# Performance work log

Measured on AMD Instinct MI355X. Metric: run time of the kernel, lower is better.

The kernel has to match this reference:

```python
import jax, jax.numpy as jnp
import numpy as np

N_NODES = 50000
N_EDGES = 800000
EMB = 128
HID = [128, 128]
OUT = 64
CE = 8  # stand-in for CROSS_ENTROPY_INDEXES: first 8 output columns get sigmoid


def _linear_params(key, d_in, d_out):
    k1, k2 = jax.random.split(key)
    s = 1.0 / np.sqrt(d_in)
    w = jax.random.uniform(k1, (d_in, d_out), minval=-s, maxval=s, dtype=jnp.float32)
    b = jax.random.uniform(k2, (d_out,), minval=-s, maxval=s, dtype=jnp.float32)
    return w, b


def setup_inputs() -> dict:
    key = jax.random.key(0)
    ks = jax.random.split(key, 16)
    z = jax.random.normal(ks[0], (N_NODES, EMB), dtype=jnp.float32)
    edge_index = jax.random.randint(ks[1], (2, N_EDGES), 0, N_NODES, dtype=jnp.int64)
    # SAGEConv params: neighbor weight (with bias) + root weight
    w1_n, b1 = _linear_params(ks[2], EMB, HID[0])
    w1_r, _ = _linear_params(ks[3], EMB, HID[0])
    w2_n, b2 = _linear_params(ks[4], HID[0], HID[1])
    w2_r, _ = _linear_params(ks[5], HID[0], HID[1])
    wf_n, bf = _linear_params(ks[6], HID[1], OUT)
    wf_r, _ = _linear_params(ks[7], HID[1], OUT)
    # initial residual linears: emb -> hid[1], emb -> out
    w_res1, b_res1 = _linear_params(ks[8], EMB, HID[1])
    w_res2, b_res2 = _linear_params(ks[9], EMB, OUT)
    return dict(z=z, edge_index=edge_index,
                w1_n=w1_n, w1_r=w1_r, b1=b1,
                w2_n=w2_n, w2_r=w2_r, b2=b2,
                wf_n=wf_n, wf_r=wf_r, bf=bf,
                w_res1=w_res1, b_res1=b_res1,
                w_res2=w_res2, b_res2=b_res2)


def _sage(x, src, dst, w_n, w_r, b, n_nodes):
    # mean-aggregate neighbor features at target nodes, then affine combine with root
    msg = x[src]                                        # [E, d]
    agg = jax.ops.segment_sum(msg, dst, num_segments=n_nodes)
    deg = jax.ops.segment_sum(jnp.ones_like(dst, dtype=x.dtype), dst, num_segments=n_nodes)
    mean = agg / jnp.maximum(deg, 1.0)[:, None]
    return mean @ w_n + x @ w_r + b


def reference(z, edge_index, w1_n, w1_r, b1, w2_n, w2_r, b2, wf_n, wf_r, bf,
              w_res1, b_res1, w_res2, b_res2):
    n = z.shape[0]
    src, dst = edge_index[0], edge_index[1]
    h = jax.nn.relu(_sage(z, src, dst, w1_n, w1_r, b1, n))
    # mid layer (dropout is identity in eval) + initial residual
    h = jax.nn.relu(_sage(h, src, dst, w2_n, w2_r, b2, n))
    h = h + (z @ w_res1 + b_res1)
    # final conv + final residual
    h = _sage(h, src, dst, wf_n, wf_r, bf, n)
    h = h + (z @ w_res2 + b_res2)
    # sigmoid on cross-entropy columns
    h = h.at[:, :CE].set(jax.nn.sigmoid(h[:, :CE]))
    return h
```

## Files before the change

### kernel.cpp

```cpp
#include <hip/hip_runtime.h>
#include <hip/hip_bf16.h>
#include <math.h>

#define NN 50000
#define NE 800000
#define NB 391
#define EPB 6250

typedef short bf16x8 __attribute__((ext_vector_type(8)));
typedef float f32x4 __attribute__((ext_vector_type(4)));
typedef unsigned short us4 __attribute__((ext_vector_type(4)));
typedef unsigned short us8 __attribute__((ext_vector_type(8)));
typedef unsigned int u32x4 __attribute__((ext_vector_type(4)));

__device__ __forceinline__ float bf2f(unsigned short u) {
  union { unsigned int i; float f; } x; x.i = ((unsigned int)u) << 16; return x.f;
}
__device__ __forceinline__ unsigned short f2bf(float f) {
  union { float f; unsigned int i; } x; x.f = f;
  unsigned int i = x.i;
  unsigned int r = i + 0x7FFF + ((i >> 16) & 1);
  return (unsigned short)(r >> 16);
}
__device__ __forceinline__ us4 pack4(f32x4 v) {
  us4 o; o[0] = f2bf(v[0]); o[1] = f2bf(v[1]); o[2] = f2bf(v[2]); o[3] = f2bf(v[3]);
  return o;
}

__global__ __launch_bounds__(256) void bhist_kernel(const int* __restrict__ dstn,
                                                    int* __restrict__ bhist) {
  __shared__ int h[NB];
  for (int i = threadIdx.x; i < NB; i += 256) h[i] = 0;
  __syncthreads();
  int e0 = blockIdx.x * EPB;
  for (int i = threadIdx.x; i < EPB; i += 256)
    atomicAdd(&h[dstn[e0 + i] >> 7], 1);
  __syncthreads();
  for (int i = threadIdx.x; i < NB; i += 256)
    if (h[i]) atomicAdd(&bhist[i], h[i]);
}

__global__ __launch_bounds__(512) void bscan_kernel(const int* __restrict__ bhist,
                                                    int* __restrict__ bucket_off,
                                                    int* __restrict__ gcur) {
  __shared__ int s[512];
  int t = threadIdx.x;
  int v = (t < NB) ? bhist[t] : 0;
  s[t] = v; __syncthreads();
  for (int off = 1; off < 512; off <<= 1) {
    int x = (t >= off) ? s[t - off] : 0;
    __syncthreads();
    s[t] += x;
    __syncthreads();
  }
  if (t < NB) { bucket_off[t] = s[t] - v; gcur[t] = 0; }
  if (t == NB - 1) bucket_off[NB] = s[t];
}

__global__ __launch_bounds__(256) void bscat_kernel(const int* __restrict__ srcn,
                                                    const int* __restrict__ dstn,
                                                    const int* __restrict__ bucket_off,
                                                    int* __restrict__ gcur,
                                                    unsigned long long* __restrict__ ebuf) {
  __shared__ int hist[NB];
  __shared__ int base[NB];
  for (int i = threadIdx.x; i < NB; i += 256) hist[i] = 0;
  __syncthreads();
  int e0 = blockIdx.x * EPB;
  for (int i = threadIdx.x; i < EPB; i += 256)
    atomicAdd(&hist[dstn[e0 + i] >> 7], 1);
  __syncthreads();
  for (int i = threadIdx.x; i < NB; i += 256) {
    int c = hist[i];
    base[i] = c ? (bucket_off[i] + atomicAdd(&gcur[i], c)) : 0;
  }
  __syncthreads();
  for (int i = threadIdx.x; i < EPB; i += 256) {
    int s = srcn[e0 + i], d = dstn[e0 + i];
    int b = d >> 7;
    int pos = atomicSub(&hist[b], 1) - 1;
    ebuf[(size_t)base[b] + pos] = ((unsigned long long)(unsigned)d << 32) | (unsigned)s;
  }
}

__global__ __launch_bounds__(256) void bfill_kernel(const unsigned long long* __restrict__ ebuf,
                                                    const int* __restrict__ bucket_off,
                                                    int* __restrict__ rowoff,
                                                    int* __restrict__ csr) {
  int b = blockIdx.x;
  int bo = bucket_off[b], cnt = bucket_off[b + 1] - bo;
  __shared__ int ndeg[128], noff[128];
  int t = threadIdx.x;
  if (t < 128) ndeg[t] = 0;
  __syncthreads();
  for (int i = t; i < cnt; i += 256)
    atomicAdd(&ndeg[(int)(ebuf[bo + i] >> 32) & 127], 1);
  __syncthreads();
  if (t < 128) noff[t] = ndeg[t];
  __syncthreads();
  for (int off = 1; off < 128; off <<= 1) {
    int x = 0;
    if (t < 128 && t >= off) x = noff[t - off];
    __syncthreads();
    if (t < 128 && t >= off) noff[t] += x;
    __syncthreads();
  }
  if (t < 128) {
    int ex = noff[t] - ndeg[t];
    noff[t] = ex;
    int node = b * 128 + t;
    if (node < NN) rowoff[node] = bo + ex;
  }
  if (b == NB - 1 && t == 0) rowoff[NN] = NE;
  __syncthreads();
  for (int i = t; i < cnt; i += 256) {
    unsigned long long e = ebuf[bo + i];
    int dl = (int)(e >> 32) & 127;
    int pos = atomicSub(&ndeg[dl], 1) - 1;
    csr[bo + noff[dl] + pos] = (int)(unsigned)e;
  }
}

__global__ void prep_kernel(const float* __restrict__ w1n, const float* __restrict__ w1r,
                            const float* __restrict__ w2n, const float* __restrict__ w2r,
                            const float* __restrict__ wfn, const float* __restrict__ wfr,
                            const float* __restrict__ wr1, const float* __restrict__ wr2,
                            unsigned short* __restrict__ Bp1, unsigned short* __restrict__ Bp2,
                            unsigned short* __restrict__ Bp3) {
  int g = blockIdx.x * 256 + threadIdx.x;
  unsigned short* D; int NT, fi;
  int which;
  if      (g < 10240) { fi = g;         D = Bp1; NT = 20; which = 1; }
  else if (g < 14336) { fi = g - 10240; D = Bp2; NT = 8;  which = 2; }
  else if (g < 16384) { fi = g - 14336; D = Bp3; NT = 4;  which = 3; }
  else return;
  int lane = fi & 63, t = fi >> 6;
  int nt = t % NT, k0i = t / NT;
  int m = lane & 15, q = lane >> 4;
  int kb = k0i * 32 + q * 8;
  int n = nt * 16 + m;
  int hi = (kb >= 128);
  int k0_ = kb - (hi ? 128 : 0);
  const float* W = nullptr; int Nseg = 128; int nn = n;
  if (which == 1) {
    if (n < 128)      { W = hi ? w1r : w1n; nn = n; Nseg = 128; }
    else if (n < 256) { W = hi ? wr1 : nullptr; nn = n - 128; Nseg = 128; }
    else              { W = hi ? wr2 : nullptr; nn = n - 256; Nseg = 64; }
  } else if (which == 2) { W = hi ? w2r : w2n; Nseg = 128; }
  else                   { W = hi ? wfr : wfn; Nseg = 64; }
  unsigned short o[8];
#pragma unroll
  for (int j = 0; j < 8; j++)
    o[j] = W ? f2bf(W[(size_t)(k0_ + j) * Nseg + nn]) : (unsigned short)0;
  *(us8*)(D + (size_t)fi * 8) = *(const us8*)o;
}

__global__ void convz_kernel(const float* __restrict__ z, unsigned short* __restrict__ A1) {
  int i = blockIdx.x * 256 + threadIdx.x;
  if (i >= NN * 128 / 4) return;
  int i4 = i * 4;
  int row = i4 >> 7, c = i4 & 127;
  float4 v = *(const float4*)(z + i4);
  us4 o = { f2bf(v.x), f2bf(v.y), f2bf(v.z), f2bf(v.w) };
  *(us4*)(A1 + (size_t)row * 256 + 128 + c) = o;
}

__global__ __launch_bounds__(256) void agg_kernel(const unsigned short* __restrict__ feat, int fstride,
                                                  unsigned short* __restrict__ outm, int ostride,
                                                  const int* __restrict__ rowoff,
                                                  const int* __restrict__ csr) {
  int wave = threadIdx.x >> 6, lane = threadIdx.x & 63;
  int node = blockIdx.x * 4 + wave;
  if (node >= NN) return;
  int beg = rowoff[node], end = rowoff[node + 1];
  int g = lane >> 4;
  int c = (lane & 15) << 3;
  float a[8];
#pragma unroll
  for (int i = 0; i < 8; i++) a[i] = 0.f;
  int j = beg + g;
  for (; j + 12 < end; j += 16) {
    int s0 = csr[j];
    int s1 = csr[j + 4];
    int s2 = csr[j + 8];
    int s3 = csr[j + 12];
    u32x4 v0 = *(const u32x4*)(feat + (size_t)s0 * fstride + c);
    u32x4 v1 = *(const u32x4*)(feat + (size_t)s1 * fstride + c);
    u32x4 v2 = *(const u32x4*)(feat + (size_t)s2 * fstride + c);
    u32x4 v3 = *(const u32x4*)(feat + (size_t)s3 * fstride + c);
#pragma unroll
    for (int i = 0; i < 4; i++) {
      a[2*i]   += bf2f((unsigned short)(v0[i] & 0xffff)) + bf2f((unsigned short)(v1[i] & 0xffff))
                + bf2f((unsigned short)(v2[i] & 0xffff)) + bf2f((unsigned short)(v3[i] & 0xffff));
      a[2*i+1] += bf2f((unsigned short)(v0[i] >> 16)) + bf2f((unsigned short)(v1[i] >> 16))
                + bf2f((unsigned short)(v2[i] >> 16)) + bf2f((unsigned short)(v3[i] >> 16));
    }
  }
  for (; j < end; j += 4) {
    int s0 = csr[j];
    u32x4 v0 = *(const u32x4*)(feat + (size_t)s0 * fstride + c);
#pragma unroll
    for (int i = 0; i < 4; i++) {
      a[2*i]   += bf2f((unsigned short)(v0[i] & 0xffff));
      a[2*i+1] += bf2f((unsigned short)(v0[i] >> 16));
    }
  }
#pragma unroll
  for (int i = 0; i < 8; i++) {
    a[i] += __shfl_xor(a[i], 16, 64);
    a[i] += __shfl_xor(a[i], 32, 64);
  }
  if (g == 0) {
    float inv = 1.f / fmaxf((float)(end - beg), 1.f);
    unsigned int o[4];
#pragma unroll
    for (int i = 0; i < 4; i++)
      o[i] = ((unsigned int)f2bf(a[2*i+1] * inv) << 16) | f2bf(a[2*i] * inv);
    *(u32x4*)(outm + (size_t)node * ostride + c) = *(const u32x4*)o;
  }
}

__global__ __launch_bounds__(256) void gemm1_kernel(
    const unsigned short* __restrict__ A,
    const unsigned short* __restrict__ Bp,
    const float* __restrict__ b1, const float* __restrict__ br1, const float* __restrict__ br2,
    unsigned short* __restrict__ h1out,
    unsigned short* __restrict__ res1, unsigned short* __restrict__ res2)
{
  const int NT = 20;
  int wave = threadIdx.x >> 6, lane = threadIdx.x & 63;
  int row0 = blockIdx.x * 64 + wave * 16;
  int m = lane & 15, q = lane >> 4;
  int ybase = blockIdx.y * 10;
  f32x4 acc[10];
#pragma unroll
  for (int i = 0; i < 10; i++) acc[i] = (f32x4){0.f, 0.f, 0.f, 0.f};
  const unsigned short* arow = A + (size_t)(row0 + m) * 256 + q * 8;
  bf16x8 af[8];
#pragma unroll
  for (int k0i = 0; k0i < 8; ++k0i) af[k0i] = *(const bf16x8*)(arow + k0i * 32);
#pragma unroll
  for (int k0i = 0; k0i < 8; ++k0i) {
    const unsigned short* bk = Bp + ((size_t)k0i * NT + ybase) * 512 + lane * 8;
#pragma unroll
    for (int s = 0; s < 10; ++s) {
      bf16x8 bfr = *(const bf16x8*)(bk + s * 512);
      acc[s] = __builtin_amdgcn_mfma_f32_16x16x32_bf16(bfr, af[k0i], acc[s], 0, 0, 0);
    }
  }
  int row = row0 + m;
  if (row >= NN) return;
  int cb = q * 4;
#pragma unroll
  for (int s = 0; s < 10; ++s) {
    int nt = ybase + s;
    f32x4 v = acc[s];
    if (nt < 8) {
      int col = nt * 16 + cb;
      float4 bb = *(const float4*)(b1 + col);
      v[0] = fmaxf(v[0] + bb.x, 0.f); v[1] = fmaxf(v[1] + bb.y, 0.f);
      v[2] = fmaxf(v[2] + bb.z, 0.f); v[3] = fmaxf(v[3] + bb.w, 0.f);
      *(us4*)(h1out + (size_t)row * 256 + col) = pack4(v);
    } else if (nt < 16) {
      int col = (nt - 8) * 16 + cb;
      float4 bb = *(const float4*)(br1 + col);
      v[0] += bb.x; v[1] += bb.y; v[2] += bb.z; v[3] += bb.w;
      *(us4*)(res1 + (size_t)row * 128 + col) = pack4(v);
    } else {
      int col = (nt - 16) * 16 + cb;
      float4 bb = *(const float4*)(br2 + col);
      v[0] += bb.x; v[1] += bb.y; v[2] += bb.z; v[3] += bb.w;
      *(us4*)(res2 + (size_t)row * 64 + col) = pack4(v);
    }
  }
}

template <int NTT>
__global__ __launch_bounds__(256) void gemm23_kernel(
    const unsigned short* __restrict__ A,
    const unsigned short* __restrict__ Bp,
    const float* __restrict__ bias,
    const unsigned short* __restrict__ res, int res_stride,
    unsigned short* __restrict__ out_bf,
    float* __restrict__ out_f, int of_stride,
    int relu, int sig8)
{
  int wave = threadIdx.x >> 6, lane = threadIdx.x & 63;
  int row0 = blockIdx.x * 64 + wave * 16;
  int m = lane & 15, q = lane >> 4;
  int ybase = blockIdx.y * 4;
  f32x4 acc[4];
#pragma unroll
  for (int i = 0; i < 4; i++) acc[i] = (f32x4){0.f, 0.f, 0.f, 0.f};
  const unsigned short* arow = A + (size_t)(row0 + m) * 256 + q * 8;
  bf16x8 af[8];
#pragma unroll
  for (int k0i = 0; k0i < 8; ++k0i) af[k0i] = *(const bf16x8*)(arow + k0i * 32);
#pragma unroll
  for (int k0i = 0; k0i < 8; ++k0i) {
    const unsigned short* bk = Bp + ((size_t)k0i * NTT + ybase) * 512 + lane * 8;
#pragma unroll
    for (int s = 0; s < 4; ++s) {
      bf16x8 bfr = *(const bf16x8*)(bk + s * 512);
      acc[s] = __builtin_amdgcn_mfma_f32_16x16x32_bf16(bfr, af[k0i], acc[s], 0, 0, 0);
    }
  }
  int row = row0 + m;
  if (row >= NN) return;
  int cb = q * 4;
#pragma unroll
  for (int s = 0; s < 4; ++s) {
    int col = (ybase + s) * 16 + cb;
    f32x4 v = acc[s];
    float4 bb = *(const float4*)(bias + col);
    v[0] += bb.x; v[1] += bb.y; v[2] += bb.z; v[3] += bb.w;
    if (relu) {
#pragma unroll
      for (int r = 0; r < 4; r++) v[r] = fmaxf(v[r], 0.f);
    }
    if (res) {
      us4 rv = *(const us4*)(res + (size_t)row * res_stride + col);
#pragma unroll
      for (int r = 0; r < 4; r++) v[r] += bf2f(rv[r]);
    }
    if (sig8 && col < 8) {
#pragma unroll
      for (int r = 0; r < 4; r++) v[r] = 1.f / (1.f + __expf(-v[r]));
    }
    if (out_bf) *(us4*)(out_bf + (size_t)row * 256 + col) = pack4(v);
    if (out_f) {
      float4 o = { v[0], v[1], v[2], v[3] };
      *(float4*)(out_f + (size_t)row * of_stride + col) = o;
    }
  }
}

extern "C" void kernel_launch(void* const* d_in, const int* in_sizes, int n_in,
                              void* d_out, int out_size, void* d_ws, size_t ws_size,
                              hipStream_t stream) {
  const float* z   = (const float*)d_in[0];
  const int*   edge = (const int*)d_in[1];
  const int*   srcn = edge;
  const int*   dstn = edge + NE;
  const float* w1n = (const float*)d_in[2];
  const float* w1r = (const float*)d_in[3];
  const float* b1  = (const float*)d_in[4];
  const float* w2n = (const float*)d_in[5];
  const float* w2r = (const float*)d_in[6];
  const float* b2  = (const float*)d_in[7];
  const float* wfn = (const float*)d_in[8];
  const float* wfr = (const float*)d_in[9];
  const float* bfb = (const float*)d_in[10];
  const float* wr1 = (const float*)d_in[11];
  const float* br1 = (const float*)d_in[12];
  const float* wr2 = (const float*)d_in[13];
  const float* br2 = (const float*)d_in[14];
  float* out = (float*)d_out;

  char* p = (char*)d_ws;
  auto alloc = [&](size_t bytes) { char* r = p; p += (bytes + 255) & ~255ull; return r; };
  int* rowoff = (int*)alloc((size_t)(NN + 1) * 4);
  int* bhist  = (int*)alloc((size_t)NB * 4);
  int* bucket_off = (int*)alloc((size_t)(NB + 1) * 4);
  int* gcur   = (int*)alloc((size_t)NB * 4);
  int* csr    = (int*)alloc((size_t)NE * 4);
  unsigned short* A1 = (unsigned short*)alloc((size_t)NN * 256 * 2);
  unsigned short* A2 = (unsigned short*)alloc((size_t)NN * 256 * 2);
  unsigned short* res1 = (unsigned short*)alloc((size_t)NN * 128 * 2);
  unsigned short* res2 = (unsigned short*)alloc((size_t)NN * 64 * 2);
  unsigned short* Bp1 = (unsigned short*)alloc(10240 * 8 * 2);
  unsigned short* Bp2 = (unsigned short*)alloc(4096 * 8 * 2);
  unsigned short* Bp3 = (unsigned short*)alloc(2048 * 8 * 2);
  unsigned short* A3 = A1;
  unsigned long long* ebuf = (unsigned long long*)res1;

  hipMemsetAsync(bhist, 0, (size_t)NB * 4, stream);
  bhist_kernel<<<128, 256, 0, stream>>>(dstn, bhist);
  bscan_kernel<<<1, 512, 0, stream>>>(bhist, bucket_off, gcur);
  bscat_kernel<<<128, 256, 0, stream>>>(srcn, dstn, bucket_off, gcur, ebuf);
  bfill_kernel<<<NB, 256, 0, stream>>>(ebuf, bucket_off, rowoff, csr);

  prep_kernel<<<64, 256, 0, stream>>>(w1n, w1r, w2n, w2r, wfn, wfr, wr1, wr2, Bp1, Bp2, Bp3);
  convz_kernel<<<(NN * 128 / 4 + 255) / 256, 256, 0, stream>>>(z, A1);

  const int gx = (NN + 63) / 64;
  const int agg_blocks = (NN + 3) / 4;

  agg_kernel<<<agg_blocks, 256, 0, stream>>>(A1 + 128, 256, A1, 256, rowoff, csr);
  gemm1_kernel<<<dim3(gx, 2), 256, 0, stream>>>(A1, Bp1, b1, br1, br2, A2 + 128, res1, res2);

  agg_kernel<<<agg_blocks, 256, 0, stream>>>(A2 + 128, 256, A2, 256, rowoff, csr);
  gemm23_kernel<8><<<dim3(gx, 2), 256, 0, stream>>>(A2, Bp2, b2, res1, 128,
      A3 + 128, nullptr, 0, 1, 0);

  agg_kernel<<<agg_blocks, 256, 0, stream>>>(A3 + 128, 256, A3, 256, rowoff, csr);
  gemm23_kernel<4><<<dim3(gx, 1), 256, 0, stream>>>(A3, Bp3, bfb, res2, 64,
      nullptr, out, 64, 0, 1);
}
```

Before: 308.6 us.

## Stage GEMM weight tiles in LDS and reorder grid so column tiles vary fastest

The GEMM kernels now copy each block's slice of the packed weight matrix into shared memory once, and the MFMA loop reads B fragments from LDS instead of from global memory per wave. The grid is transposed so blockIdx.x picks the column-tile group and blockIdx.y the row block. Adjacent blocks therefore share the same A rows, which should improve L2 reuse of activations. gemm1 also splits 20 tiles into 4 groups of 5 instead of 2 groups of 10. The changes add a cooperative load, a barrier and LDS use (up to 40KB per block), and gemm1 launches more blocks that each reload their A rows.

```diff
diff --git a/kernel.cpp b/kernel.cpp
--- a/kernel.cpp
+++ b/kernel.cpp
@@ -227,23 +227,32 @@
     unsigned short* __restrict__ h1out,
     unsigned short* __restrict__ res1, unsigned short* __restrict__ res2)
 {
-  const int NT = 20;
-  int wave = threadIdx.x >> 6, lane = threadIdx.x & 63;
-  int row0 = blockIdx.x * 64 + wave * 16;
+  const int NT = 20, TILES = 5;
+  __shared__ unsigned short Bs[TILES * 8 * 512];
+  int tid = threadIdx.x;
+  int wave = tid >> 6, lane = tid & 63;
+  int ybase = blockIdx.x * TILES;
+#pragma unroll
+  for (int i = tid; i < TILES * 64 * 8; i += 256) {
+    int k0i = i / (TILES * 64), r = i % (TILES * 64);
+    *(us8*)(Bs + (size_t)k0i * TILES * 512 + (size_t)r * 8) =
+        *(const us8*)(Bp + ((size_t)k0i * NT + ybase) * 512 + (size_t)r * 8);
+  }
+  int row0 = blockIdx.y * 64 + wave * 16;
   int m = lane & 15, q = lane >> 4;
-  int ybase = blockIdx.y * 10;
-  f32x4 acc[10];
-#pragma unroll
-  for (int i = 0; i < 10; i++) acc[i] = (f32x4){0.f, 0.f, 0.f, 0.f};
   const unsigned short* arow = A + (size_t)(row0 + m) * 256 + q * 8;
   bf16x8 af[8];
 #pragma unroll
   for (int k0i = 0; k0i < 8; ++k0i) af[k0i] = *(const bf16x8*)(arow + k0i * 32);
+  __syncthreads();
+  f32x4 acc[TILES];
+#pragma unroll
+  for (int i = 0; i < TILES; i++) acc[i] = (f32x4){0.f, 0.f, 0.f, 0.f};
 #pragma unroll
   for (int k0i = 0; k0i < 8; ++k0i) {
-    const unsigned short* bk = Bp + ((size_t)k0i * NT + ybase) * 512 + lane * 8;
-#pragma unroll
-    for (int s = 0; s < 10; ++s) {
+    const unsigned short* bk = Bs + (size_t)k0i * TILES * 512 + lane * 8;
+#pragma unroll
+    for (int s = 0; s < TILES; ++s) {
       bf16x8 bfr = *(const bf16x8*)(bk + s * 512);
       acc[s] = __builtin_amdgcn_mfma_f32_16x16x32_bf16(bfr, af[k0i], acc[s], 0, 0, 0);
     }
@@ -252,7 +261,7 @@
   if (row >= NN) return;
   int cb = q * 4;
 #pragma unroll
-  for (int s = 0; s < 10; ++s) {
+  for (int s = 0; s < TILES; ++s) {
     int nt = ybase + s;
     f32x4 v = acc[s];
     if (nt < 8) {
@@ -285,22 +294,32 @@
     float* __restrict__ out_f, int of_stride,
     int relu, int sig8)
 {
-  int wave = threadIdx.x >> 6, lane = threadIdx.x & 63;
-  int row0 = blockIdx.x * 64 + wave * 16;
+  const int TILES = 4;
+  __shared__ unsigned short Bs[TILES * 8 * 512];
+  int tid = threadIdx.x;
+  int wave = tid >> 6, lane = tid & 63;
+  int ybase = blockIdx.x * TILES;
+#pragma unroll
+  for (int i = tid; i < TILES * 64 * 8; i += 256) {
+    int k0i = i / (TILES * 64), r = i % (TILES * 64);
+    *(us8*)(Bs + (size_t)k0i * TILES * 512 + (size_t)r * 8) =
+        *(const us8*)(Bp + ((size_t)k0i * NTT + ybase) * 512 + (size_t)r * 8);
+  }
+  int row0 = blockIdx.y * 64 + wave * 16;
   int m = lane & 15, q = lane >> 4;
-  int ybase = blockIdx.y * 4;
-  f32x4 acc[4];
-#pragma unroll
-  for (int i = 0; i < 4; i++) acc[i] = (f32x4){0.f, 0.f, 0.f, 0.f};
   const unsigned short* arow = A + (size_t)(row0 + m) * 256 + q * 8;
   bf16x8 af[8];
 #pragma unroll
   for (int k0i = 0; k0i < 8; ++k0i) af[k0i] = *(const bf16x8*)(arow + k0i * 32);
+  __syncthreads();
+  f32x4 acc[TILES];
+#pragma unroll
+  for (int i = 0; i < TILES; i++) acc[i] = (f32x4){0.f, 0.f, 0.f, 0.f};
 #pragma unroll
   for (int k0i = 0; k0i < 8; ++k0i) {
-    const unsigned short* bk = Bp + ((size_t)k0i * NTT + ybase) * 512 + lane * 8;
-#pragma unroll
-    for (int s = 0; s < 4; ++s) {
+    const unsigned short* bk = Bs + (size_t)k0i * TILES * 512 + lane * 8;
+#pragma unroll
+    for (int s = 0; s < TILES; ++s) {
       bf16x8 bfr = *(const bf16x8*)(bk + s * 512);
       acc[s] = __builtin_amdgcn_mfma_f32_16x16x32_bf16(bfr, af[k0i], acc[s], 0, 0, 0);
     }
@@ -309,7 +328,7 @@
   if (row >= NN) return;
   int cb = q * 4;
 #pragma unroll
-  for (int s = 0; s < 4; ++s) {
+  for (int s = 0; s < TILES; ++s) {
     int col = (ybase + s) * 16 + cb;
     f32x4 v = acc[s];
     float4 bb = *(const float4*)(bias + col);
@@ -383,17 +402,17 @@
   prep_kernel<<<64, 256, 0, stream>>>(w1n, w1r, w2n, w2r, wfn, wfr, wr1, wr2, Bp1, Bp2, Bp3);
   convz_kernel<<<(NN * 128 / 4 + 255) / 256, 256, 0, stream>>>(z, A1);
 
-  const int gx = (NN + 63) / 64;
+  const int gy = (NN + 63) / 64;
   const int agg_blocks = (NN + 3) / 4;
 
   agg_kernel<<<agg_blocks, 256, 0, stream>>>(A1 + 128, 256, A1, 256, rowoff, csr);
-  gemm1_kernel<<<dim3(gx, 2), 256, 0, stream>>>(A1, Bp1, b1, br1, br2, A2 + 128, res1, res2);
+  gemm1_kernel<<<dim3(4, gy), 256, 0, stream>>>(A1, Bp1, b1, br1, br2, A2 + 128, res1, res2);
 
   agg_kernel<<<agg_blocks, 256, 0, stream>>>(A2 + 128, 256, A2, 256, rowoff, csr);
-  gemm23_kernel<8><<<dim3(gx, 2), 256, 0, stream>>>(A2, Bp2, b2, res1, 128,
+  gemm23_kernel<8><<<dim3(2, gy), 256, 0, stream>>>(A2, Bp2, b2, res1, 128,
       A3 + 128, nullptr, 0, 1, 0);
 
   agg_kernel<<<agg_blocks, 256, 0, stream>>>(A3 + 128, 256, A3, 256, rowoff, csr);
-  gemm23_kernel<4><<<dim3(gx, 1), 256, 0, stream>>>(A3, Bp3, bfb, res2, 64,
+  gemm23_kernel<4><<<dim3(1, gy), 256, 0, stream>>>(A3, Bp3, bfb, res2, 64,
       nullptr, out, 64, 0, 1);
 }
```

New measurement: 297.6 us. 3.6% less time.
